# Optimization experiments

Measured on AMD Instinct MI355X. Metric: run time of the kernel, lower is better.

## Reference

```python
import jax, jax.numpy as jnp
import numpy as np

N_FEAT = 6
N_CUT = 3          # cuts per feature -> N_CUT+1 bins
NUM_LEAF = (N_CUT + 1) ** N_FEAT  # 4096
NUM_CLASS = 10
BATCH = 16384


def setup_inputs() -> dict:
    key = jax.random.key(0)
    k1, k2, k3 = jax.random.split(key, 3)
    x = jax.random.normal(k1, (BATCH, N_FEAT), dtype=jnp.float32)
    cuts = jax.random.uniform(k2, (N_FEAT, N_CUT), dtype=jnp.float32)
    leaf_score = jax.random.uniform(k3, (NUM_LEAF, NUM_CLASS), dtype=jnp.float32)
    temperature = jnp.full((1,), 0.1, dtype=jnp.float32)
    return {"x": x, "cuts": cuts, "leaf_score": leaf_score, "temperature": temperature}


def _soft_bin(x, cuts, temperature):
    # x: [B, F], cuts: [F, D] -> bins [B, F, D+1]
    F_, D = cuts.shape
    W = jnp.arange(1.0, D + 2.0, dtype=x.dtype)                      # [D+1] == linspace(1, D+1, D+1)
    sc = jnp.sort(cuts, axis=1)                                       # sort per feature
    b = jnp.cumsum(jnp.concatenate([jnp.zeros((F_, 1), x.dtype), -sc], axis=1), axis=1)  # [F, D+1]
    h = (x[:, :, None] * W[None, None, :] + b[None, :, :]) / temperature  # [B, F, D+1]
    return jax.nn.softmax(h, axis=-1)


def reference(x, cuts, leaf_score, temperature):
    t = temperature[0]
    bins = _soft_bin(x, cuts, t)                  # [B, F, D+1]
    B = x.shape[0]
    # sequential kron outer-products over features (fixed small loop)
    leaf = bins[:, 0, :]                           # [B, D+1]
    for f in range(1, N_FEAT):
        leaf = jnp.einsum('bj,bk->bjk', leaf, bins[:, f, :]).reshape(B, -1)
    return leaf @ leaf_score                       # [B, NUM_CLASS]
```

## Files before the change

### kernel.cpp

```cpp
#include <hip/hip_runtime.h>
#include <hip/hip_bf16.h>

#define NCLASS 10
#define B_BYTES 81920
#define BINS_OFF 81920
#define BINS_STRIDE 28
#define LDS_BYTES (B_BYTES + 64 * BINS_STRIDE * 4)

typedef __bf16 bf16x8 __attribute__((ext_vector_type(8)));
typedef __bf16 bf16x2 __attribute__((ext_vector_type(2)));
typedef float  f32x4  __attribute__((ext_vector_type(4)));
typedef float  f32x2  __attribute__((ext_vector_type(2)));

__device__ __forceinline__ unsigned pack2(float lo, float hi) {
    bf16x2 p = {(__bf16)lo, (__bf16)hi};
    return __builtin_bit_cast(unsigned, p);
}

__device__ __forceinline__ bf16x8 mk_a(const f32x2* t8v, float base) {
    bf16x8 a;
    #pragma unroll
    for (int i = 0; i < 4; ++i) {
        f32x2 p = t8v[i] * base;
        a[2 * i]     = (__bf16)p[0];
        a[2 * i + 1] = (__bf16)p[1];
    }
    return a;
}

__launch_bounds__(1024, 4)
__global__ void dndt_mfma(const float* __restrict__ x,
                          const float* __restrict__ cuts,
                          const float* __restrict__ ls,
                          const float* __restrict__ temperature,
                          float* __restrict__ out)
{
    __shared__ __attribute__((aligned(16))) char LS[LDS_BYTES];
    const int tid = threadIdx.x;

    {
        const float4* ls4 = (const float4*)ls;
        #pragma unroll
        for (int pp = 0; pp < 2; ++pp) {
            const int j = pp * 1024 + tid;
            float4 f0 = ls4[5 * j + 0];
            float4 f1 = ls4[5 * j + 1];
            float4 f2 = ls4[5 * j + 2];
            float4 f3 = ls4[5 * j + 3];
            float4 f4 = ls4[5 * j + 4];
            float k0[10] = {f0.x, f0.y, f0.z, f0.w, f1.x, f1.y, f1.z, f1.w, f2.x, f2.y};
            float k1[10] = {f2.z, f2.w, f3.x, f3.y, f3.z, f3.w, f4.x, f4.y, f4.z, f4.w};
            #pragma unroll
            for (int n = 0; n < NCLASS; ++n) {
                unsigned addr = ((unsigned)n << 13) +
                                (((unsigned)(j << 2)) ^ (((unsigned)(n & 7)) << 4));
                *(unsigned*)(LS + addr) = pack2(k0[n], k1[n]);
            }
        }
    }

    float* BINS = (float*)(LS + BINS_OFF);
    const float sc = 1.44269504088896f / temperature[0];
    if (tid < 512) {
        const int rl = tid >> 3, f = tid & 7;
        if (f < 6) {
            const int grow = (blockIdx.x << 6) + rl;
            float xv = x[grow * 6 + f];
            float c0 = cuts[f * 3 + 0], c1 = cuts[f * 3 + 1], cv = cuts[f * 3 + 2];
            float lo01 = fminf(c0, c1), hi01 = fmaxf(c0, c1);
            float s2 = fmaxf(hi01, cv), mh = fminf(hi01, cv);
            float s0 = fminf(lo01, mh), s1 = fmaxf(lo01, mh);
            float h0 = xv * sc;
            float h1 = fmaf(xv, 2.f * sc, -s0 * sc);
            float h2 = fmaf(xv, 3.f * sc, (-s0 - s1) * sc);
            float h3 = fmaf(xv, 4.f * sc, (-s0 - s1 - s2) * sc);
            float m = fmaxf(fmaxf(h0, h1), fmaxf(h2, h3));
            float e0 = exp2f(h0 - m), e1 = exp2f(h1 - m);
            float e2 = exp2f(h2 - m), e3 = exp2f(h3 - m);
            float rs = 1.f / (e0 + e1 + e2 + e3);
            f32x4 b = {e0 * rs, e1 * rs, e2 * rs, e3 * rs};
            *(f32x4*)&BINS[rl * BINS_STRIDE + f * 4] = b;
        }
    }

    __syncthreads();

    const int wave = tid >> 6, lane = tid & 63;
    const int rt = wave >> 2;
    const int ks = wave & 3;
    const int r  = lane & 15;
    const int kg = lane >> 4;
    const int rl = rt * 16 + r;

    const float* BR = &BINS[rl * BINS_STRIDE];
    f32x4 b0v = *(const f32x4*)&BR[0];
    f32x4 b1v = *(const f32x4*)&BR[4];
    f32x4 b2v = *(const f32x4*)&BR[8];
    f32x4 b3v = *(const f32x4*)&BR[12];
    f32x4 b4v = *(const f32x4*)&BR[16];
    f32x4 b5v = *(const f32x4*)&BR[20];

    const int kgl = kg & 1, kgh = kg >> 1;
    f32x2 t8v[4];
    {
        float b4a = b4v[kgl * 2 + 0], b4b = b4v[kgl * 2 + 1];
        t8v[0] = (f32x2){b4a * b5v[0], b4a * b5v[1]};
        t8v[1] = (f32x2){b4a * b5v[2], b4a * b5v[3]};
        t8v[2] = (f32x2){b4b * b5v[0], b4b * b5v[1]};
        t8v[3] = (f32x2){b4b * b5v[2], b4b * b5v[3]};
    }
    const float b3e = b3v[kgh];
    const float b3o = b3v[2 + kgh];
    const float b0  = b0v[ks];

    const int n_eff = (r < NCLASS) ? r : 9;
    const unsigned base0 = ((unsigned)n_eff << 13) +
                           ((((unsigned)kg) << 4) ^ ((((unsigned)n_eff) & 3u) << 4));
    const unsigned c6 = (((unsigned)n_eff) >> 2) & 1u;
    const int be = (int)(base0 + (c6 << 6)) + ks * 2048;
    const int bo = (int)(base0 + ((1u - c6) << 6)) + ks * 2048;

    f32x4 acc = {0.f, 0.f, 0.f, 0.f};
    #pragma unroll
    for (int m1 = 0; m1 < 4; ++m1) {
        const float b01 = b0 * b1v[m1];
        #pragma unroll
        for (int m2 = 0; m2 < 4; ++m2) {
            const float b012 = b01 * b2v[m2];
            const int off = (m1 * 4 + m2) * 128;
            {
                bf16x8 a = mk_a(t8v, b012 * b3e);
                bf16x8 b = *(const bf16x8*)(LS + (be + off));
                acc = __builtin_amdgcn_mfma_f32_16x16x32_bf16(a, b, acc, 0, 0, 0);
            }
            {
                bf16x8 a = mk_a(t8v, b012 * b3o);
                bf16x8 b = *(const bf16x8*)(LS + (bo + off));
                acc = __builtin_amdgcn_mfma_f32_16x16x32_bf16(a, b, acc, 0, 0, 0);
            }
        }
    }

    __syncthreads();
    float* red = (float*)LS;
    *(f32x4*)&red[((size_t)wave * 64 + lane) * 4] = acc;
    __syncthreads();
    if (ks == 0) {
        f32x4 p1 = *(f32x4*)&red[(((size_t)rt * 4 + 1) * 64 + lane) * 4];
        f32x4 p2 = *(f32x4*)&red[(((size_t)rt * 4 + 2) * 64 + lane) * 4];
        f32x4 p3 = *(f32x4*)&red[(((size_t)rt * 4 + 3) * 64 + lane) * 4];
        f32x4 tot = acc + p1 + p2 + p3;
        if (r < NCLASS) {
            #pragma unroll
            for (int q = 0; q < 4; ++q) {
                int grow = (blockIdx.x << 6) + (rt << 4) + kg * 4 + q;
                out[(size_t)grow * NCLASS + r] = tot[q];
            }
        }
    }
}

extern "C" void kernel_launch(void* const* d_in, const int* in_sizes, int n_in,
                              void* d_out, int out_size, void* d_ws, size_t ws_size,
                              hipStream_t stream) {
    const float* x           = (const float*)d_in[0];
    const float* cuts        = (const float*)d_in[1];
    const float* leaf_score  = (const float*)d_in[2];
    const float* temperature = (const float*)d_in[3];
    float* out = (float*)d_out;
    dndt_mfma<<<256, 1024, 0, stream>>>(x, cuts, leaf_score, temperature, out);
}
```

Before: 12.06 us.

## Compute soft bins per wave in registers and reuse LDS B tiles across two row tiles

```diff
diff --git a/kernel.cpp b/kernel.cpp
--- a/kernel.cpp
+++ b/kernel.cpp
@@ -3,9 +3,6 @@
 
 #define NCLASS 10
 #define B_BYTES 81920
-#define BINS_OFF 81920
-#define BINS_STRIDE 28
-#define LDS_BYTES (B_BYTES + 64 * BINS_STRIDE * 4)
 
 typedef __bf16 bf16x8 __attribute__((ext_vector_type(8)));
 typedef __bf16 bf16x2 __attribute__((ext_vector_type(2)));
@@ -28,6 +25,38 @@
     return a;
 }
 
+__device__ __forceinline__ void row_params(
+    const float xv[6], const float off1[6], const float off2[6], const float off3[6],
+    float sc, int kgl, int kgh, int l0, int l1hi,
+    float& b01a, float& b01b, f32x4& b2v, float& b3e, float& b3o, f32x2 t8v[4])
+{
+    float bins[6][4];
+    #pragma unroll
+    for (int f = 0; f < 6; ++f) {
+        float h0 = xv[f] * sc;
+        float h1 = fmaf(xv[f], 2.f * sc, off1[f]);
+        float h2 = fmaf(xv[f], 3.f * sc, off2[f]);
+        float h3 = fmaf(xv[f], 4.f * sc, off3[f]);
+        float m = fmaxf(fmaxf(h0, h1), fmaxf(h2, h3));
+        float e0 = exp2f(h0 - m), e1 = exp2f(h1 - m);
+        float e2 = exp2f(h2 - m), e3 = exp2f(h3 - m);
+        float rs = 1.f / (e0 + e1 + e2 + e3);
+        bins[f][0] = e0 * rs; bins[f][1] = e1 * rs;
+        bins[f][2] = e2 * rs; bins[f][3] = e3 * rs;
+    }
+    float b0s = bins[0][l0];
+    b01a = b0s * bins[1][l1hi];
+    b01b = b0s * bins[1][l1hi + 1];
+    b2v = *(f32x4*)&bins[2][0];
+    b3e = bins[3][kgh];
+    b3o = bins[3][2 + kgh];
+    float b4a = bins[4][kgl * 2 + 0], b4b = bins[4][kgl * 2 + 1];
+    t8v[0] = (f32x2){b4a * bins[5][0], b4a * bins[5][1]};
+    t8v[1] = (f32x2){b4a * bins[5][2], b4a * bins[5][3]};
+    t8v[2] = (f32x2){b4b * bins[5][0], b4b * bins[5][1]};
+    t8v[3] = (f32x2){b4b * bins[5][2], b4b * bins[5][3]};
+}
+
 __launch_bounds__(1024, 4)
 __global__ void dndt_mfma(const float* __restrict__ x,
                           const float* __restrict__ cuts,
@@ -35,125 +64,105 @@
                           const float* __restrict__ temperature,
                           float* __restrict__ out)
 {
-    __shared__ __attribute__((aligned(16))) char LS[LDS_BYTES];
+    __shared__ __attribute__((aligned(16))) char LS[B_BYTES];
     const int tid = threadIdx.x;
+    const int w = tid >> 6, lane = tid & 63;
+    const int r = lane & 15, kg = lane >> 4;
+    const int kc = w & 7;
+    const int rtg = w >> 3;
+
+    const int rl0 = rtg * 32 + r;
+    const int grow0 = (blockIdx.x << 6) + rl0;
+    const float2* x2 = (const float2*)x;
+    float2 xa0 = x2[grow0 * 3 + 0], xa1 = x2[grow0 * 3 + 1], xa2 = x2[grow0 * 3 + 2];
+    float2 xb0 = x2[(grow0 + 16) * 3 + 0], xb1 = x2[(grow0 + 16) * 3 + 1],
+           xb2 = x2[(grow0 + 16) * 3 + 2];
+
+    const float4* ls4 = (const float4*)ls;
+    float4 g[10];
+    #pragma unroll
+    for (int i = 0; i < 10; ++i) g[i] = ls4[10 * tid + i];
+
+    const float sc = 1.44269504088896f / temperature[0];
+    float off1[6], off2[6], off3[6];
+    #pragma unroll
+    for (int f = 0; f < 6; ++f) {
+        float c0 = cuts[f * 3 + 0], c1 = cuts[f * 3 + 1], cv = cuts[f * 3 + 2];
+        float lo01 = fminf(c0, c1), hi01 = fmaxf(c0, c1);
+        float s2 = fmaxf(hi01, cv), mh = fminf(hi01, cv);
+        float s0 = fminf(lo01, mh), s1 = fmaxf(lo01, mh);
+        off1[f] = -s0 * sc;
+        off2[f] = (-s0 - s1) * sc;
+        off3[f] = (-s0 - s1 - s2) * sc;
+    }
+
+    const int kgl = kg & 1, kgh = kg >> 1;
+    const int l0 = kc >> 1, l1hi = (kc & 1) << 1;
+    float b01a0, b01b0, b3e0, b3o0, b01a1, b01b1, b3e1, b3o1;
+    f32x4 b2v0, b2v1;
+    f32x2 t80[4], t81[4];
+    {
+        float xv0[6] = {xa0.x, xa0.y, xa1.x, xa1.y, xa2.x, xa2.y};
+        row_params(xv0, off1, off2, off3, sc, kgl, kgh, l0, l1hi,
+                   b01a0, b01b0, b2v0, b3e0, b3o0, t80);
+        float xv1[6] = {xb0.x, xb0.y, xb1.x, xb1.y, xb2.x, xb2.y};
+        row_params(xv1, off1, off2, off3, sc, kgl, kgh, l0, l1hi,
+                   b01a1, b01b1, b2v1, b3e1, b3o1, t81);
+    }
 
     {
-        const float4* ls4 = (const float4*)ls;
+        float v[40];
         #pragma unroll
-        for (int pp = 0; pp < 2; ++pp) {
-            const int j = pp * 1024 + tid;
-            float4 f0 = ls4[5 * j + 0];
-            float4 f1 = ls4[5 * j + 1];
-            float4 f2 = ls4[5 * j + 2];
-            float4 f3 = ls4[5 * j + 3];
-            float4 f4 = ls4[5 * j + 4];
-            float k0[10] = {f0.x, f0.y, f0.z, f0.w, f1.x, f1.y, f1.z, f1.w, f2.x, f2.y};
-            float k1[10] = {f2.z, f2.w, f3.x, f3.y, f3.z, f3.w, f4.x, f4.y, f4.z, f4.w};
-            #pragma unroll
-            for (int n = 0; n < NCLASS; ++n) {
-                unsigned addr = ((unsigned)n << 13) +
-                                (((unsigned)(j << 2)) ^ (((unsigned)(n & 7)) << 4));
-                *(unsigned*)(LS + addr) = pack2(k0[n], k1[n]);
-            }
+        for (int i = 0; i < 10; ++i) {
+            v[4 * i] = g[i].x; v[4 * i + 1] = g[i].y;
+            v[4 * i + 2] = g[i].z; v[4 * i + 3] = g[i].w;
         }
-    }
-
-    float* BINS = (float*)(LS + BINS_OFF);
-    const float sc = 1.44269504088896f / temperature[0];
-    if (tid < 512) {
-        const int rl = tid >> 3, f = tid & 7;
-        if (f < 6) {
-            const int grow = (blockIdx.x << 6) + rl;
-            float xv = x[grow * 6 + f];
-            float c0 = cuts[f * 3 + 0], c1 = cuts[f * 3 + 1], cv = cuts[f * 3 + 2];
-            float lo01 = fminf(c0, c1), hi01 = fmaxf(c0, c1);
-            float s2 = fmaxf(hi01, cv), mh = fminf(hi01, cv);
-            float s0 = fminf(lo01, mh), s1 = fmaxf(lo01, mh);
-            float h0 = xv * sc;
-            float h1 = fmaf(xv, 2.f * sc, -s0 * sc);
-            float h2 = fmaf(xv, 3.f * sc, (-s0 - s1) * sc);
-            float h3 = fmaf(xv, 4.f * sc, (-s0 - s1 - s2) * sc);
-            float m = fmaxf(fmaxf(h0, h1), fmaxf(h2, h3));
-            float e0 = exp2f(h0 - m), e1 = exp2f(h1 - m);
-            float e2 = exp2f(h2 - m), e3 = exp2f(h3 - m);
-            float rs = 1.f / (e0 + e1 + e2 + e3);
-            f32x4 b = {e0 * rs, e1 * rs, e2 * rs, e3 * rs};
-            *(f32x4*)&BINS[rl * BINS_STRIDE + f * 4] = b;
+        #pragma unroll
+        for (int n = 0; n < NCLASS; ++n) {
+            uint2 dw = { pack2(v[n], v[10 + n]), pack2(v[20 + n], v[30 + n]) };
+            unsigned addr = ((unsigned)n << 13) +
+                            (((unsigned)(tid << 3)) ^ (((unsigned)(n & 7)) << 4));
+            *(uint2*)(LS + addr) = dw;
         }
     }
 
     __syncthreads();
 
-    const int wave = tid >> 6, lane = tid & 63;
-    const int rt = wave >> 2;
-    const int ks = wave & 3;
-    const int r  = lane & 15;
-    const int kg = lane >> 4;
-    const int rl = rt * 16 + r;
-
-    const float* BR = &BINS[rl * BINS_STRIDE];
-    f32x4 b0v = *(const f32x4*)&BR[0];
-    f32x4 b1v = *(const f32x4*)&BR[4];
-    f32x4 b2v = *(const f32x4*)&BR[8];
-    f32x4 b3v = *(const f32x4*)&BR[12];
-    f32x4 b4v = *(const f32x4*)&BR[16];
-    f32x4 b5v = *(const f32x4*)&BR[20];
-
-    const int kgl = kg & 1, kgh = kg >> 1;
-    f32x2 t8v[4];
-    {
-        float b4a = b4v[kgl * 2 + 0], b4b = b4v[kgl * 2 + 1];
-        t8v[0] = (f32x2){b4a * b5v[0], b4a * b5v[1]};
-        t8v[1] = (f32x2){b4a * b5v[2], b4a * b5v[3]};
-        t8v[2] = (f32x2){b4b * b5v[0], b4b * b5v[1]};
-        t8v[3] = (f32x2){b4b * b5v[2], b4b * b5v[3]};
-    }
-    const float b3e = b3v[kgh];
-    const float b3o = b3v[2 + kgh];
-    const float b0  = b0v[ks];
-
     const int n_eff = (r < NCLASS) ? r : 9;
-    const unsigned base0 = ((unsigned)n_eff << 13) +
+    const unsigned base0 = ((unsigned)n_eff << 13) + ((unsigned)kc << 10) +
                            ((((unsigned)kg) << 4) ^ ((((unsigned)n_eff) & 3u) << 4));
     const unsigned c6 = (((unsigned)n_eff) >> 2) & 1u;
-    const int be = (int)(base0 + (c6 << 6)) + ks * 2048;
-    const int bo = (int)(base0 + ((1u - c6) << 6)) + ks * 2048;
+    const char* pe = LS + base0 + (c6 << 6);
+    const char* po = LS + base0 + ((1u - c6) << 6);
 
-    f32x4 acc = {0.f, 0.f, 0.f, 0.f};
+    f32x4 acc0 = {0.f, 0.f, 0.f, 0.f}, acc1 = {0.f, 0.f, 0.f, 0.f};
     #pragma unroll
-    for (int m1 = 0; m1 < 4; ++m1) {
-        const float b01 = b0 * b1v[m1];
-        #pragma unroll
-        for (int m2 = 0; m2 < 4; ++m2) {
-            const float b012 = b01 * b2v[m2];
-            const int off = (m1 * 4 + m2) * 128;
-            {
-                bf16x8 a = mk_a(t8v, b012 * b3e);
-                bf16x8 b = *(const bf16x8*)(LS + (be + off));
-                acc = __builtin_amdgcn_mfma_f32_16x16x32_bf16(a, b, acc, 0, 0, 0);
-            }
-            {
-                bf16x8 a = mk_a(t8v, b012 * b3o);
-                bf16x8 b = *(const bf16x8*)(LS + (bo + off));
-                acc = __builtin_amdgcn_mfma_f32_16x16x32_bf16(a, b, acc, 0, 0, 0);
-            }
-        }
+    for (int s2 = 0; s2 < 8; ++s2) {
+        bf16x8 Be = *(const bf16x8*)(pe + s2 * 128);
+        bf16x8 Bo = *(const bf16x8*)(po + s2 * 128);
+        float m0 = b2v0[s2 & 3] * ((s2 >> 2) ? b01b0 : b01a0);
+        float m1 = b2v1[s2 & 3] * ((s2 >> 2) ? b01b1 : b01a1);
+        acc0 = __builtin_amdgcn_mfma_f32_16x16x32_bf16(mk_a(t80, m0 * b3e0), Be, acc0, 0, 0, 0);
+        acc1 = __builtin_amdgcn_mfma_f32_16x16x32_bf16(mk_a(t81, m1 * b3e1), Be, acc1, 0, 0, 0);
+        acc0 = __builtin_amdgcn_mfma_f32_16x16x32_bf16(mk_a(t80, m0 * b3o0), Bo, acc0, 0, 0, 0);
+        acc1 = __builtin_amdgcn_mfma_f32_16x16x32_bf16(mk_a(t81, m1 * b3o1), Bo, acc1, 0, 0, 0);
     }
 
     __syncthreads();
-    float* red = (float*)LS;
-    *(f32x4*)&red[((size_t)wave * 64 + lane) * 4] = acc;
+    f32x4* red = (f32x4*)LS;
+    red[(w * 2 + 0) * 64 + lane] = acc0;
+    red[(w * 2 + 1) * 64 + lane] = acc1;
     __syncthreads();
-    if (ks == 0) {
-        f32x4 p1 = *(f32x4*)&red[(((size_t)rt * 4 + 1) * 64 + lane) * 4];
-        f32x4 p2 = *(f32x4*)&red[(((size_t)rt * 4 + 2) * 64 + lane) * 4];
-        f32x4 p3 = *(f32x4*)&red[(((size_t)rt * 4 + 3) * 64 + lane) * 4];
-        f32x4 tot = acc + p1 + p2 + p3;
+    if (w < 4) {
+        const int rt = w;
+        const int sbase = (rt >> 1) * 16 + (rt & 1);
+        f32x4 tot = red[sbase * 64 + lane];
+        #pragma unroll
+        for (int k8 = 1; k8 < 8; ++k8) tot += red[(sbase + 2 * k8) * 64 + lane];
         if (r < NCLASS) {
             #pragma unroll
             for (int q = 0; q < 4; ++q) {
-                int grow = (blockIdx.x << 6) + (rt << 4) + kg * 4 + q;
+                int grow = (blockIdx.x << 6) + rt * 16 + kg * 4 + q;
                 out[(size_t)grow * NCLASS + r] = tot[q];
             }
         }
```

New measurement: 19.42 us. +61.0%, slower.

## Split K across eight waves with two row tiles sharing each B fragment

Applied to the files above, without the earlier changes.

```diff
diff --git a/kernel.cpp b/kernel.cpp
--- a/kernel.cpp
+++ b/kernel.cpp
@@ -85,75 +85,77 @@
 
     __syncthreads();
 
-    const int wave = tid >> 6, lane = tid & 63;
-    const int rt = wave >> 2;
-    const int ks = wave & 3;
+    const int w = tid >> 6, lane = tid & 63;
     const int r  = lane & 15;
     const int kg = lane >> 4;
-    const int rl = rt * 16 + r;
-
-    const float* BR = &BINS[rl * BINS_STRIDE];
-    f32x4 b0v = *(const f32x4*)&BR[0];
-    f32x4 b1v = *(const f32x4*)&BR[4];
-    f32x4 b2v = *(const f32x4*)&BR[8];
-    f32x4 b3v = *(const f32x4*)&BR[12];
-    f32x4 b4v = *(const f32x4*)&BR[16];
-    f32x4 b5v = *(const f32x4*)&BR[20];
+    const int kc = w & 7;
+    const int rtg = w >> 3;
+    const int rl0 = rtg * 32 + r;
 
     const int kgl = kg & 1, kgh = kg >> 1;
-    f32x2 t8v[4];
-    {
+    const int l0 = kc >> 1, l1hi = (kc & 1) << 1;
+
+    float b01a0, b01b0, b3e0, b3o0, b01a1, b01b1, b3e1, b3o1;
+    f32x4 b2v0, b2v1;
+    f32x2 t80[4], t81[4];
+    #pragma unroll
+    for (int rr = 0; rr < 2; ++rr) {
+        const float* BR = &BINS[(rl0 + rr * 16) * BINS_STRIDE];
+        f32x4 b0v = *(const f32x4*)&BR[0];
+        f32x4 b1v = *(const f32x4*)&BR[4];
+        f32x4 b2v = *(const f32x4*)&BR[8];
+        f32x4 b3v = *(const f32x4*)&BR[12];
+        f32x4 b4v = *(const f32x4*)&BR[16];
+        f32x4 b5v = *(const f32x4*)&BR[20];
+        float b0s = b0v[l0];
+        float ba = b0s * b1v[l1hi], bb = b0s * b1v[l1hi + 1];
+        float be = b3v[kgh], bo = b3v[2 + kgh];
         float b4a = b4v[kgl * 2 + 0], b4b = b4v[kgl * 2 + 1];
-        t8v[0] = (f32x2){b4a * b5v[0], b4a * b5v[1]};
-        t8v[1] = (f32x2){b4a * b5v[2], b4a * b5v[3]};
-        t8v[2] = (f32x2){b4b * b5v[0], b4b * b5v[1]};
-        t8v[3] = (f32x2){b4b * b5v[2], b4b * b5v[3]};
+        f32x2 t0 = {b4a * b5v[0], b4a * b5v[1]};
+        f32x2 t1 = {b4a * b5v[2], b4a * b5v[3]};
+        f32x2 t2 = {b4b * b5v[0], b4b * b5v[1]};
+        f32x2 t3 = {b4b * b5v[2], b4b * b5v[3]};
+        if (rr == 0) { b01a0 = ba; b01b0 = bb; b2v0 = b2v; b3e0 = be; b3o0 = bo;
+                       t80[0] = t0; t80[1] = t1; t80[2] = t2; t80[3] = t3; }
+        else         { b01a1 = ba; b01b1 = bb; b2v1 = b2v; b3e1 = be; b3o1 = bo;
+                       t81[0] = t0; t81[1] = t1; t81[2] = t2; t81[3] = t3; }
     }
-    const float b3e = b3v[kgh];
-    const float b3o = b3v[2 + kgh];
-    const float b0  = b0v[ks];
 
     const int n_eff = (r < NCLASS) ? r : 9;
-    const unsigned base0 = ((unsigned)n_eff << 13) +
+    const unsigned base0 = ((unsigned)n_eff << 13) + ((unsigned)kc << 10) +
                            ((((unsigned)kg) << 4) ^ ((((unsigned)n_eff) & 3u) << 4));
     const unsigned c6 = (((unsigned)n_eff) >> 2) & 1u;
-    const int be = (int)(base0 + (c6 << 6)) + ks * 2048;
-    const int bo = (int)(base0 + ((1u - c6) << 6)) + ks * 2048;
+    const char* pe = LS + base0 + (c6 << 6);
+    const char* po = LS + base0 + ((1u - c6) << 6);
 
-    f32x4 acc = {0.f, 0.f, 0.f, 0.f};
+    f32x4 acc0 = {0.f, 0.f, 0.f, 0.f}, acc1 = {0.f, 0.f, 0.f, 0.f};
     #pragma unroll
-    for (int m1 = 0; m1 < 4; ++m1) {
-        const float b01 = b0 * b1v[m1];
-        #pragma unroll
-        for (int m2 = 0; m2 < 4; ++m2) {
-            const float b012 = b01 * b2v[m2];
-            const int off = (m1 * 4 + m2) * 128;
-            {
-                bf16x8 a = mk_a(t8v, b012 * b3e);
-                bf16x8 b = *(const bf16x8*)(LS + (be + off));
-                acc = __builtin_amdgcn_mfma_f32_16x16x32_bf16(a, b, acc, 0, 0, 0);
-            }
-            {
-                bf16x8 a = mk_a(t8v, b012 * b3o);
-                bf16x8 b = *(const bf16x8*)(LS + (bo + off));
-                acc = __builtin_amdgcn_mfma_f32_16x16x32_bf16(a, b, acc, 0, 0, 0);
-            }
-        }
+    for (int s2 = 0; s2 < 8; ++s2) {
+        bf16x8 Be = *(const bf16x8*)(pe + s2 * 128);
+        bf16x8 Bo = *(const bf16x8*)(po + s2 * 128);
+        float m0 = b2v0[s2 & 3] * ((s2 >> 2) ? b01b0 : b01a0);
+        float m1 = b2v1[s2 & 3] * ((s2 >> 2) ? b01b1 : b01a1);
+        acc0 = __builtin_amdgcn_mfma_f32_16x16x32_bf16(mk_a(t80, m0 * b3e0), Be, acc0, 0, 0, 0);
+        acc1 = __builtin_amdgcn_mfma_f32_16x16x32_bf16(mk_a(t81, m1 * b3e1), Be, acc1, 0, 0, 0);
+        acc0 = __builtin_amdgcn_mfma_f32_16x16x32_bf16(mk_a(t80, m0 * b3o0), Bo, acc0, 0, 0, 0);
+        acc1 = __builtin_amdgcn_mfma_f32_16x16x32_bf16(mk_a(t81, m1 * b3o1), Bo, acc1, 0, 0, 0);
     }
 
     __syncthreads();
-    float* red = (float*)LS;
-    *(f32x4*)&red[((size_t)wave * 64 + lane) * 4] = acc;
+    f32x4* red = (f32x4*)LS;
+    red[(w * 2 + 0) * 64 + lane] = acc0;
+    red[(w * 2 + 1) * 64 + lane] = acc1;
     __syncthreads();
-    if (ks == 0) {
-        f32x4 p1 = *(f32x4*)&red[(((size_t)rt * 4 + 1) * 64 + lane) * 4];
-        f32x4 p2 = *(f32x4*)&red[(((size_t)rt * 4 + 2) * 64 + lane) * 4];
-        f32x4 p3 = *(f32x4*)&red[(((size_t)rt * 4 + 3) * 64 + lane) * 4];
-        f32x4 tot = acc + p1 + p2 + p3;
+    if (w < 4) {
+        const int rt = w;
+        const int sbase = (rt >> 1) * 16 + (rt & 1);
+        f32x4 tot = red[sbase * 64 + lane];
+        #pragma unroll
+        for (int k8 = 1; k8 < 8; ++k8) tot += red[(sbase + 2 * k8) * 64 + lane];
         if (r < NCLASS) {
             #pragma unroll
             for (int q = 0; q < 4; ++q) {
-                int grow = (blockIdx.x << 6) + (rt << 4) + kg * 4 + q;
+                int grow = (blockIdx.x << 6) + rt * 16 + kg * 4 + q;
                 out[(size_t)grow * NCLASS + r] = tot[q];
             }
         }
```

Measured after the change: 12.19 us. Within noise of the previous version (+1.0%).
